# Kernel optimization log

Measured on AMD Instinct MI355X. Metric: run time of the kernel, lower is better.

The kernel has to match this reference:

```python
import jax, jax.numpy as jnp
import numpy as np

EMBED = 1024
HEADS = 16
HEAD_DIM = EMBED // HEADS


def setup_inputs() -> dict:
    key = jax.random.key(0)
    ks = jax.random.split(key, 5)
    s = 0.02
    x = jax.random.normal(ks[0], (2, 2048, EMBED), dtype=jnp.float32)
    W_qkv = jax.random.normal(ks[1], (EMBED, 3 * EMBED), dtype=jnp.float32) * s
    b_qkv = jnp.zeros((3 * EMBED,), dtype=jnp.float32)
    W_proj = jax.random.normal(ks[2], (EMBED, EMBED), dtype=jnp.float32) * s
    b_proj = jnp.zeros((EMBED,), dtype=jnp.float32)
    return {"x": x, "W_qkv": W_qkv, "b_qkv": b_qkv, "W_proj": W_proj, "b_proj": b_proj}


def reference(x, W_qkv, b_qkv, W_proj, b_proj):
    B, N, _ = x.shape
    scale = HEAD_DIM ** -0.5
    qkv = x @ W_qkv + b_qkv                     # [B,N,3E]
    qkv = qkv.reshape(B, N, 3, HEADS, HEAD_DIM)
    q = qkv[:, :, 0].transpose(0, 2, 1, 3) * scale  # [B,H,N,D]
    k = qkv[:, :, 1].transpose(0, 2, 1, 3)
    v = qkv[:, :, 2].transpose(0, 2, 1, 3)
    attn = jnp.einsum('bhnd,bhmd->bhnm', q, k)  # [B,H,N,N]
    attn = jax.nn.softmax(attn, axis=-1)
    out = jnp.einsum('bhnm,bhmd->bhnd', attn, v)  # [B,H,N,D]
    out = out.transpose(0, 2, 1, 3).reshape(B, N, HEADS * HEAD_DIM)
    return out @ W_proj + b_proj
```

## Files before the change

### kernel.cpp

```cpp
#include <hip/hip_runtime.h>
#include <hip/hip_bf16.h>
#include <stdint.h>

typedef unsigned short u16;
typedef __bf16 bf16x8 __attribute__((ext_vector_type(8)));
typedef float f32x4 __attribute__((ext_vector_type(4)));

__device__ __forceinline__ u16 f2bf(float f) {
    union { float f; unsigned u; } x; x.f = f;
    unsigned u = x.u;
    u += 0x7FFFu + ((u >> 16) & 1u);
    return (u16)(u >> 16);
}

typedef __attribute__((address_space(1))) void gvoid;
typedef __attribute__((address_space(3))) void lvoid;
__device__ __forceinline__ void gl2lds16(const void* g, void* l) {
    __builtin_amdgcn_global_load_lds((gvoid*)g, (lvoid*)l, 16, 0, 0);
}

__global__ __launch_bounds__(256) void prep_kernel(
    const float* __restrict__ x, u16* __restrict__ xb,
    const float* __restrict__ Wqkv, u16* __restrict__ wqkvT,
    const float* __restrict__ Wproj, u16* __restrict__ wprojT)
{
    __shared__ u16 tile[64][65];
    const int blk = blockIdx.x;
    const int tid = threadIdx.x;

    if (blk < 2048) {
        const size_t i = ((size_t)blk * 256 + tid) * 8;
        float4 a = *(const float4*)(x + i);
        float4 b = *(const float4*)(x + i + 4);
        ushort4 oa, ob;
        oa.x = f2bf(a.x); oa.y = f2bf(a.y); oa.z = f2bf(a.z); oa.w = f2bf(a.w);
        ob.x = f2bf(b.x); ob.y = f2bf(b.y); ob.z = f2bf(b.z); ob.w = f2bf(b.w);
        *(ushort4*)(xb + i) = oa;
        *(ushort4*)(xb + i + 4) = ob;
        return;
    }
    const float* in; u16* out; int rows, cols, bx, by;
    if (blk < 2816) { int t = blk - 2048; in = Wqkv;  out = wqkvT;  rows = 1024; cols = 3072; bx = t % 48; by = t / 48; }
    else            { int t = blk - 2816; in = Wproj; out = wprojT; rows = 1024; cols = 1024; bx = t % 16; by = t / 16; }
#pragma unroll
    for (int i = 0; i < 16; i++) {
        int e = i * 256 + tid;
        int r = e >> 6, c = e & 63;
        tile[r][c] = f2bf(in[(size_t)(by * 64 + r) * cols + bx * 64 + c]);
    }
    __syncthreads();
#pragma unroll
    for (int i = 0; i < 16; i++) {
        int e = i * 256 + tid;
        int r = e >> 6, c = e & 63;
        out[(size_t)(bx * 64 + r) * rows + by * 64 + c] = tile[c][r];
    }
}

__global__ __launch_bounds__(256) void transpose_v(
    const u16* __restrict__ in, u16* __restrict__ out)
{
    __shared__ u16 tile[64][65];
    const int bh = blockIdx.y;
    const int t0 = blockIdx.x * 64;
    const u16* ip = in + ((size_t)bh * 2048 + t0) * 64;
    u16* op = out + (size_t)bh * 64 * 2048 + t0;
    const int tid = threadIdx.x;
#pragma unroll
    for (int i = 0; i < 16; i++) {
        int e = i * 256 + tid;
        int r = e >> 6, c = e & 63;
        tile[r][c] = ip[(size_t)r * 64 + c];
    }
    __syncthreads();
#pragma unroll
    for (int i = 0; i < 16; i++) {
        int e = i * 256 + tid;
        int d = e >> 6, tt = e & 63;
        op[(size_t)d * 2048 + tt] = tile[tt][d];
    }
}

__global__ __launch_bounds__(256) void gemm_qkv(
    const u16* __restrict__ A, const u16* __restrict__ Bt,
    const float* __restrict__ bias,
    u16* __restrict__ q, u16* __restrict__ ko, u16* __restrict__ vo)
{
    constexpr int K = 1024;
    __shared__ __align__(16) u16 sA[128 * 64];
    __shared__ __align__(16) u16 sB[128 * 64];
    const int tid = threadIdx.x;
    const int wave = tid >> 6, lane = tid & 63;
    const int quad = lane >> 4, l16 = lane & 15;
    const int wm = (wave >> 1) * 64, wn = (wave & 1) * 64;
    const int m0 = blockIdx.y * 128, n0 = blockIdx.x * 128;
    const int srow = lane >> 3;
    const int scol = (lane & 7) * 8;

    f32x4 acc[4][4];
#pragma unroll
    for (int i = 0; i < 4; i++)
#pragma unroll
        for (int j = 0; j < 4; j++)
#pragma unroll
            for (int r = 0; r < 4; r++) acc[i][j][r] = 0.f;

    for (int kt = 0; kt < K; kt += 64) {
        __syncthreads();
#pragma unroll
        for (int t = 0; t < 4; t++) {
            int rb = wave * 32 + t * 8;
            gl2lds16(A  + (size_t)(m0 + rb + srow) * K + kt + scol, &sA[rb * 64]);
            gl2lds16(Bt + (size_t)(n0 + rb + srow) * K + kt + scol, &sB[rb * 64]);
        }
        __syncthreads();
#pragma unroll
        for (int kk = 0; kk < 64; kk += 32) {
            bf16x8 af[4], bfr[4];
#pragma unroll
            for (int t = 0; t < 4; t++) {
                af[t]  = *(const bf16x8*)&sA[(wm + t * 16 + l16) * 64 + kk + quad * 8];
                bfr[t] = *(const bf16x8*)&sB[(wn + t * 16 + l16) * 64 + kk + quad * 8];
            }
#pragma unroll
            for (int i = 0; i < 4; i++)
#pragma unroll
                for (int j = 0; j < 4; j++)
                    acc[i][j] = __builtin_amdgcn_mfma_f32_16x16x32_bf16(
                        af[i], bfr[j], acc[i][j], 0, 0, 0);
        }
    }

    const float QSCALE = 0.18033688011112042f;
#pragma unroll
    for (int i = 0; i < 4; i++) {
#pragma unroll
        for (int j = 0; j < 4; j++) {
            int n = n0 + wn + j * 16 + l16;
            float bv = bias[n];
            int which = n >> 10, rem = n & 1023;
            int h = rem >> 6, d = rem & 63;
#pragma unroll
            for (int r = 0; r < 4; r++) {
                int m = m0 + wm + i * 16 + quad * 4 + r;
                float v = acc[i][j][r] + bv;
                int b = m >> 11, t = m & 2047;
                size_t idx = ((size_t)(b * 16 + h) * 2048 + t) * 64 + d;
                if (which == 0)
                    q[idx] = f2bf(v * QSCALE);
                else if (which == 1)
                    ko[idx] = f2bf(v);
                else
                    vo[idx] = f2bf(v);
            }
        }
    }
}

__global__ __launch_bounds__(256) void attn_kernel(
    const u16* __restrict__ q, const u16* __restrict__ ko,
    const u16* __restrict__ vt, u16* __restrict__ o)
{
    __shared__ __align__(16) u16 sQ[128 * 72];
    __shared__ __align__(16) u16 sK[64 * 72];
    __shared__ __align__(16) u16 sV[80 * 72];
    __shared__ __align__(16) float sPf[128 * 68];

    const int tid = threadIdx.x;
    const int wave = tid >> 6, lane = tid & 63;
    const int quad = lane >> 4, l16 = lane & 15;

    const int lid = blockIdx.x;
    const int xcd = lid & 7, idx = lid >> 3;
    const int h = xcd * 2 + (idx & 1);
    const int b = (idx >> 1) & 1;
    const int q0 = (idx >> 2) * 128;
    const size_t bh = (size_t)(b * 16 + h);

    const u16* qp  = q  + bh * 2048 * 64;
    const u16* kp  = ko + bh * 2048 * 64;
    const u16* vtp = vt + bh * 64 * 2048;

    const int sr0 = tid >> 3;
    const int sc0 = (tid & 7) * 8;
    const int sr1 = (tid + 256) >> 3;
    const int sc1 = sc0;

#pragma unroll
    for (int i = 0; i < 4; i++) {
        int c = tid + i * 256;
        int r = c >> 3, cc = c & 7;
        *(uint4*)&sQ[r * 72 + cc * 8] =
            *(const uint4*)(qp + (size_t)(q0 + r) * 64 + cc * 8);
    }
#pragma unroll
    for (int i = 0; i < 4; i++) {
        int c = tid + i * 256;
        sV[(64 + (c >> 6)) * 72 + (c & 63)] = 0x3F80;
    }

    uint4 pk0 = *(const uint4*)(kp + (size_t)sr0 * 64 + sc0);
    uint4 pk1 = *(const uint4*)(kp + (size_t)sr1 * 64 + sc1);
    uint4 pv0 = *(const uint4*)(vtp + (size_t)sr0 * 2048 + sc0);
    uint4 pv1 = *(const uint4*)(vtp + (size_t)sr1 * 2048 + sc1);

    __syncthreads();

    bf16x8 qf[2][2];
#pragma unroll
    for (int i = 0; i < 2; i++)
#pragma unroll
        for (int k2 = 0; k2 < 2; k2++)
            qf[i][k2] = *(const bf16x8*)&sQ[(wave * 32 + i * 16 + l16) * 72 + k2 * 32 + quad * 8];

    f32x4 accO[2][4];
    f32x4 accL[2];
#pragma unroll
    for (int i = 0; i < 2; i++) {
#pragma unroll
        for (int r = 0; r < 4; r++) accL[i][r] = 0.f;
#pragma unroll
        for (int j = 0; j < 4; j++)
#pragma unroll
            for (int r = 0; r < 4; r++) accO[i][j][r] = 0.f;
    }

    for (int kt = 0; kt < 2048; kt += 64) {
        __syncthreads();
        *(uint4*)&sK[sr0 * 72 + sc0] = pk0;
        *(uint4*)&sK[sr1 * 72 + sc1] = pk1;
        *(uint4*)&sV[sr0 * 72 + sc0] = pv0;
        *(uint4*)&sV[sr1 * 72 + sc1] = pv1;
        if (kt + 64 < 2048) {
            int nt = kt + 64;
            pk0 = *(const uint4*)(kp + (size_t)(nt + sr0) * 64 + sc0);
            pk1 = *(const uint4*)(kp + (size_t)(nt + sr1) * 64 + sc1);
            pv0 = *(const uint4*)(vtp + (size_t)sr0 * 2048 + nt + sc0);
            pv1 = *(const uint4*)(vtp + (size_t)sr1 * 2048 + nt + sc1);
        }
        __syncthreads();

        f32x4 S[2][4];
#pragma unroll
        for (int i = 0; i < 2; i++)
#pragma unroll
            for (int j = 0; j < 4; j++)
#pragma unroll
                for (int r = 0; r < 4; r++) S[i][j][r] = 0.f;
#pragma unroll
        for (int k2 = 0; k2 < 2; k2++) {
            int kk = k2 * 32;
#pragma unroll
            for (int j = 0; j < 4; j++) {
                bf16x8 bk = *(const bf16x8*)&sK[(j * 16 + l16) * 72 + kk + quad * 8];
                S[0][j] = __builtin_amdgcn_mfma_f32_16x16x32_bf16(qf[0][k2], bk, S[0][j], 0, 0, 0);
                S[1][j] = __builtin_amdgcn_mfma_f32_16x16x32_bf16(qf[1][k2], bk, S[1][j], 0, 0, 0);
            }
        }

        float* pw = &sPf[(wave * 32 + quad * 4) * 68 + l16];
#pragma unroll
        for (int i = 0; i < 2; i++)
#pragma unroll
            for (int j = 0; j < 4; j++)
#pragma unroll
                for (int r = 0; r < 4; r++)
                    pw[(i * 16 + r) * 68 + j * 16] = __builtin_amdgcn_exp2f(S[i][j][r]);

#pragma unroll
        for (int k2 = 0; k2 < 2; k2++) {
            int kk = k2 * 32;
            bf16x8 bv[5];
#pragma unroll
            for (int j = 0; j < 5; j++)
                bv[j] = *(const bf16x8*)&sV[(j * 16 + l16) * 72 + kk + quad * 8];
#pragma unroll
            for (int i = 0; i < 2; i++) {
                const uint32_t* pr =
                    (const uint32_t*)&sPf[(wave * 32 + i * 16 + l16) * 68 + kk + quad * 8];
                uint4 w0 = *(const uint4*)pr;
                uint4 w1 = *(const uint4*)(pr + 4);
                union { uint32_t u[4]; bf16x8 v; } ap;
                ap.u[0] = __builtin_amdgcn_perm(w0.y, w0.x, 0x07060302u);
                ap.u[1] = __builtin_amdgcn_perm(w0.w, w0.z, 0x07060302u);
                ap.u[2] = __builtin_amdgcn_perm(w1.y, w1.x, 0x07060302u);
                ap.u[3] = __builtin_amdgcn_perm(w1.w, w1.z, 0x07060302u);
#pragma unroll
                for (int j = 0; j < 4; j++)
                    accO[i][j] = __builtin_amdgcn_mfma_f32_16x16x32_bf16(ap.v, bv[j], accO[i][j], 0, 0, 0);
                accL[i] = __builtin_amdgcn_mfma_f32_16x16x32_bf16(ap.v, bv[4], accL[i], 0, 0, 0);
            }
        }
    }

#pragma unroll
    for (int i = 0; i < 2; i++)
#pragma unroll
        for (int r = 0; r < 4; r++) {
            float inv = 1.f / accL[i][r];
            size_t row = (size_t)b * 2048 + q0 + wave * 32 + i * 16 + quad * 4 + r;
#pragma unroll
            for (int j = 0; j < 4; j++)
                o[row * 1024 + h * 64 + j * 16 + l16] = f2bf(accO[i][j][r] * inv);
        }
}

__global__ __launch_bounds__(256) void gemm_proj(
    const u16* __restrict__ A, const u16* __restrict__ Bt,
    const float* __restrict__ bias, float* __restrict__ out)
{
    constexpr int K = 1024;
    __shared__ __align__(16) u16 sA[128 * 64];
    __shared__ __align__(16) u16 sB[128 * 64];
    const int tid = threadIdx.x;
    const int wave = tid >> 6, lane = tid & 63;
    const int quad = lane >> 4, l16 = lane & 15;
    const int wm = (wave >> 1) * 64, wn = (wave & 1) * 64;
    const int m0 = blockIdx.y * 128, n0 = blockIdx.x * 128;
    const int srow = lane >> 3;
    const int scol = (lane & 7) * 8;

    f32x4 acc[4][4];
#pragma unroll
    for (int i = 0; i < 4; i++)
#pragma unroll
        for (int j = 0; j < 4; j++)
#pragma unroll
            for (int r = 0; r < 4; r++) acc[i][j][r] = 0.f;

    for (int kt = 0; kt < K; kt += 64) {
        __syncthreads();
#pragma unroll
        for (int t = 0; t < 4; t++) {
            int rb = wave * 32 + t * 8;
            gl2lds16(A  + (size_t)(m0 + rb + srow) * K + kt + scol, &sA[rb * 64]);
            gl2lds16(Bt + (size_t)(n0 + rb + srow) * K + kt + scol, &sB[rb * 64]);
        }
        __syncthreads();
#pragma unroll
        for (int kk = 0; kk < 64; kk += 32) {
            bf16x8 af[4], bfr[4];
#pragma unroll
            for (int t = 0; t < 4; t++) {
                af[t]  = *(const bf16x8*)&sA[(wm + t * 16 + l16) * 64 + kk + quad * 8];
                bfr[t] = *(const bf16x8*)&sB[(wn + t * 16 + l16) * 64 + kk + quad * 8];
            }
#pragma unroll
            for (int i = 0; i < 4; i++)
#pragma unroll
                for (int j = 0; j < 4; j++)
                    acc[i][j] = __builtin_amdgcn_mfma_f32_16x16x32_bf16(
                        af[i], bfr[j], acc[i][j], 0, 0, 0);
        }
    }

#pragma unroll
    for (int i = 0; i < 4; i++) {
#pragma unroll
        for (int j = 0; j < 4; j++) {
            int n = n0 + wn + j * 16 + l16;
            float bv = bias[n];
#pragma unroll
            for (int r = 0; r < 4; r++) {
                int m = m0 + wm + i * 16 + quad * 4 + r;
                out[(size_t)m * 1024 + n] = acc[i][j][r] + bv;
            }
        }
    }
}

extern "C" void kernel_launch(void* const* d_in, const int* in_sizes, int n_in,
                              void* d_out, int out_size, void* d_ws, size_t ws_size,
                              hipStream_t stream) {
    const float* x     = (const float*)d_in[0];
    const float* Wqkv  = (const float*)d_in[1];
    const float* bqkv  = (const float*)d_in[2];
    const float* Wproj = (const float*)d_in[3];
    const float* bproj = (const float*)d_in[4];
    float* out = (float*)d_out;
    char* ws = (char*)d_ws;

    u16* wqkvT  = (u16*)(ws);
    u16* wprojT = (u16*)(ws +  6291456);
    u16* xb     = (u16*)(ws +  8388608);
    u16* qb     = (u16*)(ws + 16777216);
    u16* kb     = (u16*)(ws + 25165824);
    u16* vtb    = (u16*)(ws + 33554432);
    u16* ob     = (u16*)(ws + 41943040);
    u16* vb     = ob;

    prep_kernel<<<dim3(3072), 256, 0, stream>>>(x, xb, Wqkv, wqkvT, Wproj, wprojT);
    gemm_qkv<<<dim3(24, 32), 256, 0, stream>>>(xb, wqkvT, bqkv, qb, kb, vb);
    transpose_v<<<dim3(32, 32), 256, 0, stream>>>(vb, vtb);
    attn_kernel<<<dim3(512), 256, 0, stream>>>(qb, kb, vtb, ob);
    gemm_proj<<<dim3(8, 32), 256, 0, stream>>>(ob, wprojT, bproj, out);
}
```

Measured before the change: 222.4 us.

## Register-prefetch GEMM tiles, XCD-aware block mapping, bf16 P in attention

```diff
diff --git a/kernel.cpp b/kernel.cpp
--- a/kernel.cpp
+++ b/kernel.cpp
@@ -11,12 +11,6 @@
     unsigned u = x.u;
     u += 0x7FFFu + ((u >> 16) & 1u);
     return (u16)(u >> 16);
-}
-
-typedef __attribute__((address_space(1))) void gvoid;
-typedef __attribute__((address_space(3))) void lvoid;
-__device__ __forceinline__ void gl2lds16(const void* g, void* l) {
-    __builtin_amdgcn_global_load_lds((gvoid*)g, (lvoid*)l, 16, 0, 0);
 }
 
 __global__ __launch_bounds__(256) void prep_kernel(
@@ -87,15 +81,21 @@
     u16* __restrict__ q, u16* __restrict__ ko, u16* __restrict__ vo)
 {
     constexpr int K = 1024;
-    __shared__ __align__(16) u16 sA[128 * 64];
-    __shared__ __align__(16) u16 sB[128 * 64];
+    __shared__ __align__(16) u16 sA[128 * 72];
+    __shared__ __align__(16) u16 sB[128 * 72];
     const int tid = threadIdx.x;
     const int wave = tid >> 6, lane = tid & 63;
     const int quad = lane >> 4, l16 = lane & 15;
     const int wm = (wave >> 1) * 64, wn = (wave & 1) * 64;
-    const int m0 = blockIdx.y * 128, n0 = blockIdx.x * 128;
-    const int srow = lane >> 3;
-    const int scol = (lane & 7) * 8;
+
+    const int lid = blockIdx.x;
+    const int xcd = lid & 7, idx = lid >> 3;
+    const int sm = xcd & 3, sn = xcd >> 2;
+    const int m0 = (sm * 8 + (idx & 7)) * 128;
+    const int n0 = (sn * 12 + (idx >> 3)) * 128;
+
+    const int srow = tid >> 3;
+    const int scol = (tid & 7) * 8;
 
     f32x4 acc[4][4];
 #pragma unroll
@@ -105,13 +105,27 @@
 #pragma unroll
             for (int r = 0; r < 4; r++) acc[i][j][r] = 0.f;
 
+    uint4 ra[4], rb[4];
+#pragma unroll
+    for (int p = 0; p < 4; p++) {
+        ra[p] = *(const uint4*)(A  + (size_t)(m0 + srow + p * 32) * K + scol);
+        rb[p] = *(const uint4*)(Bt + (size_t)(n0 + srow + p * 32) * K + scol);
+    }
+
     for (int kt = 0; kt < K; kt += 64) {
         __syncthreads();
 #pragma unroll
-        for (int t = 0; t < 4; t++) {
-            int rb = wave * 32 + t * 8;
-            gl2lds16(A  + (size_t)(m0 + rb + srow) * K + kt + scol, &sA[rb * 64]);
-            gl2lds16(Bt + (size_t)(n0 + rb + srow) * K + kt + scol, &sB[rb * 64]);
+        for (int p = 0; p < 4; p++) {
+            *(uint4*)&sA[(srow + p * 32) * 72 + scol] = ra[p];
+            *(uint4*)&sB[(srow + p * 32) * 72 + scol] = rb[p];
+        }
+        if (kt + 64 < K) {
+            int nt = kt + 64;
+#pragma unroll
+            for (int p = 0; p < 4; p++) {
+                ra[p] = *(const uint4*)(A  + (size_t)(m0 + srow + p * 32) * K + nt + scol);
+                rb[p] = *(const uint4*)(Bt + (size_t)(n0 + srow + p * 32) * K + nt + scol);
+            }
         }
         __syncthreads();
 #pragma unroll
@@ -119,8 +133,8 @@
             bf16x8 af[4], bfr[4];
 #pragma unroll
             for (int t = 0; t < 4; t++) {
-                af[t]  = *(const bf16x8*)&sA[(wm + t * 16 + l16) * 64 + kk + quad * 8];
-                bfr[t] = *(const bf16x8*)&sB[(wn + t * 16 + l16) * 64 + kk + quad * 8];
+                af[t]  = *(const bf16x8*)&sA[(wm + t * 16 + l16) * 72 + kk + quad * 8];
+                bfr[t] = *(const bf16x8*)&sB[(wn + t * 16 + l16) * 72 + kk + quad * 8];
             }
 #pragma unroll
             for (int i = 0; i < 4; i++)
@@ -145,13 +159,13 @@
                 int m = m0 + wm + i * 16 + quad * 4 + r;
                 float v = acc[i][j][r] + bv;
                 int b = m >> 11, t = m & 2047;
-                size_t idx = ((size_t)(b * 16 + h) * 2048 + t) * 64 + d;
+                size_t gi = ((size_t)(b * 16 + h) * 2048 + t) * 64 + d;
                 if (which == 0)
-                    q[idx] = f2bf(v * QSCALE);
+                    q[gi] = f2bf(v * QSCALE);
                 else if (which == 1)
-                    ko[idx] = f2bf(v);
+                    ko[gi] = f2bf(v);
                 else
-                    vo[idx] = f2bf(v);
+                    vo[gi] = f2bf(v);
             }
         }
     }
@@ -163,8 +177,8 @@
 {
     __shared__ __align__(16) u16 sQ[128 * 72];
     __shared__ __align__(16) u16 sK[64 * 72];
-    __shared__ __align__(16) u16 sV[80 * 72];
-    __shared__ __align__(16) float sPf[128 * 68];
+    __shared__ __align__(16) u16 sV[64 * 72];
+    __shared__ __align__(16) u16 sP[128 * 72];
 
     const int tid = threadIdx.x;
     const int wave = tid >> 6, lane = tid & 63;
@@ -184,7 +198,6 @@
     const int sr0 = tid >> 3;
     const int sc0 = (tid & 7) * 8;
     const int sr1 = (tid + 256) >> 3;
-    const int sc1 = sc0;
 
 #pragma unroll
     for (int i = 0; i < 4; i++) {
@@ -193,16 +206,14 @@
         *(uint4*)&sQ[r * 72 + cc * 8] =
             *(const uint4*)(qp + (size_t)(q0 + r) * 64 + cc * 8);
     }
-#pragma unroll
-    for (int i = 0; i < 4; i++) {
-        int c = tid + i * 256;
-        sV[(64 + (c >> 6)) * 72 + (c & 63)] = 0x3F80;
-    }
+
+    union { uint32_t u[4]; bf16x8 v; } ones;
+    ones.u[0] = ones.u[1] = ones.u[2] = ones.u[3] = 0x3F803F80u;
 
     uint4 pk0 = *(const uint4*)(kp + (size_t)sr0 * 64 + sc0);
-    uint4 pk1 = *(const uint4*)(kp + (size_t)sr1 * 64 + sc1);
+    uint4 pk1 = *(const uint4*)(kp + (size_t)sr1 * 64 + sc0);
     uint4 pv0 = *(const uint4*)(vtp + (size_t)sr0 * 2048 + sc0);
-    uint4 pv1 = *(const uint4*)(vtp + (size_t)sr1 * 2048 + sc1);
+    uint4 pv1 = *(const uint4*)(vtp + (size_t)sr1 * 2048 + sc0);
 
     __syncthreads();
 
@@ -228,15 +239,15 @@
     for (int kt = 0; kt < 2048; kt += 64) {
         __syncthreads();
         *(uint4*)&sK[sr0 * 72 + sc0] = pk0;
-        *(uint4*)&sK[sr1 * 72 + sc1] = pk1;
+        *(uint4*)&sK[sr1 * 72 + sc0] = pk1;
         *(uint4*)&sV[sr0 * 72 + sc0] = pv0;
-        *(uint4*)&sV[sr1 * 72 + sc1] = pv1;
+        *(uint4*)&sV[sr1 * 72 + sc0] = pv1;
         if (kt + 64 < 2048) {
             int nt = kt + 64;
             pk0 = *(const uint4*)(kp + (size_t)(nt + sr0) * 64 + sc0);
-            pk1 = *(const uint4*)(kp + (size_t)(nt + sr1) * 64 + sc1);
+            pk1 = *(const uint4*)(kp + (size_t)(nt + sr1) * 64 + sc0);
             pv0 = *(const uint4*)(vtp + (size_t)sr0 * 2048 + nt + sc0);
-            pv1 = *(const uint4*)(vtp + (size_t)sr1 * 2048 + nt + sc1);
+            pv1 = *(const uint4*)(vtp + (size_t)sr1 * 2048 + nt + sc0);
         }
         __syncthreads();
 
@@ -258,37 +269,32 @@
             }
         }
 
-        float* pw = &sPf[(wave * 32 + quad * 4) * 68 + l16];
+        u16* pw = &sP[(wave * 32 + quad * 4) * 72 + l16];
 #pragma unroll
         for (int i = 0; i < 2; i++)
 #pragma unroll
             for (int j = 0; j < 4; j++)
 #pragma unroll
-                for (int r = 0; r < 4; r++)
-                    pw[(i * 16 + r) * 68 + j * 16] = __builtin_amdgcn_exp2f(S[i][j][r]);
+                for (int r = 0; r < 4; r++) {
+                    union { float f; uint32_t u; } e;
+                    e.f = __builtin_amdgcn_exp2f(S[i][j][r]);
+                    pw[(i * 16 + r) * 72 + j * 16] = (u16)(e.u >> 16);
+                }
 
 #pragma unroll
         for (int k2 = 0; k2 < 2; k2++) {
             int kk = k2 * 32;
-            bf16x8 bv[5];
-#pragma unroll
-            for (int j = 0; j < 5; j++)
+            bf16x8 bv[4];
+#pragma unroll
+            for (int j = 0; j < 4; j++)
                 bv[j] = *(const bf16x8*)&sV[(j * 16 + l16) * 72 + kk + quad * 8];
 #pragma unroll
             for (int i = 0; i < 2; i++) {
-                const uint32_t* pr =
-                    (const uint32_t*)&sPf[(wave * 32 + i * 16 + l16) * 68 + kk + quad * 8];
-                uint4 w0 = *(const uint4*)pr;
-                uint4 w1 = *(const uint4*)(pr + 4);
-                union { uint32_t u[4]; bf16x8 v; } ap;
-                ap.u[0] = __builtin_amdgcn_perm(w0.y, w0.x, 0x07060302u);
-                ap.u[1] = __builtin_amdgcn_perm(w0.w, w0.z, 0x07060302u);
-                ap.u[2] = __builtin_amdgcn_perm(w1.y, w1.x, 0x07060302u);
-                ap.u[3] = __builtin_amdgcn_perm(w1.w, w1.z, 0x07060302u);
+                bf16x8 ap = *(const bf16x8*)&sP[(wave * 32 + i * 16 + l16) * 72 + kk + quad * 8];
 #pragma unroll
                 for (int j = 0; j < 4; j++)
-                    accO[i][j] = __builtin_amdgcn_mfma_f32_16x16x32_bf16(ap.v, bv[j], accO[i][j], 0, 0, 0);
-                accL[i] = __builtin_amdgcn_mfma_f32_16x16x32_bf16(ap.v, bv[4], accL[i], 0, 0, 0);
+                    accO[i][j] = __builtin_amdgcn_mfma_f32_16x16x32_bf16(ap, bv[j], accO[i][j], 0, 0, 0);
+                accL[i] = __builtin_amdgcn_mfma_f32_16x16x32_bf16(ap, ones.v, accL[i], 0, 0, 0);
             }
         }
     }
@@ -310,15 +316,20 @@
     const float* __restrict__ bias, float* __restrict__ out)
 {
     constexpr int K = 1024;
-    __shared__ __align__(16) u16 sA[128 * 64];
-    __shared__ __align__(16) u16 sB[128 * 64];
+    __shared__ __align__(16) u16 sA[128 * 72];
+    __shared__ __align__(16) u16 sB[128 * 72];
     const int tid = threadIdx.x;
     const int wave = tid >> 6, lane = tid & 63;
     const int quad = lane >> 4, l16 = lane & 15;
     const int wm = (wave >> 1) * 64, wn = (wave & 1) * 64;
-    const int m0 = blockIdx.y * 128, n0 = blockIdx.x * 128;
-    const int srow = lane >> 3;
-    const int scol = (lane & 7) * 8;
+
+    const int lid = blockIdx.x;
+    const int xcd = lid & 7, idx = lid >> 3;
+    const int m0 = (xcd * 4 + (idx >> 3)) * 128;
+    const int n0 = (idx & 7) * 128;
+
+    const int srow = tid >> 3;
+    const int scol = (tid & 7) * 8;
 
     f32x4 acc[4][4];
 #pragma unroll
@@ -328,13 +339,27 @@
 #pragma unroll
             for (int r = 0; r < 4; r++) acc[i][j][r] = 0.f;
 
+    uint4 ra[4], rb[4];
+#pragma unroll
+    for (int p = 0; p < 4; p++) {
+        ra[p] = *(const uint4*)(A  + (size_t)(m0 + srow + p * 32) * K + scol);
+        rb[p] = *(const uint4*)(Bt + (size_t)(n0 + srow + p * 32) * K + scol);
+    }
+
     for (int kt = 0; kt < K; kt += 64) {
         __syncthreads();
 #pragma unroll
-        for (int t = 0; t < 4; t++) {
-            int rb = wave * 32 + t * 8;
-            gl2lds16(A  + (size_t)(m0 + rb + srow) * K + kt + scol, &sA[rb * 64]);
-            gl2lds16(Bt + (size_t)(n0 + rb + srow) * K + kt + scol, &sB[rb * 64]);
+        for (int p = 0; p < 4; p++) {
+            *(uint4*)&sA[(srow + p * 32) * 72 + scol] = ra[p];
+            *(uint4*)&sB[(srow + p * 32) * 72 + scol] = rb[p];
+        }
+        if (kt + 64 < K) {
+            int nt = kt + 64;
+#pragma unroll
+            for (int p = 0; p < 4; p++) {
+                ra[p] = *(const uint4*)(A  + (size_t)(m0 + srow + p * 32) * K + nt + scol);
+                rb[p] = *(const uint4*)(Bt + (size_t)(n0 + srow + p * 32) * K + nt + scol);
+            }
         }
         __syncthreads();
 #pragma unroll
@@ -342,8 +367,8 @@
             bf16x8 af[4], bfr[4];
 #pragma unroll
             for (int t = 0; t < 4; t++) {
-                af[t]  = *(const bf16x8*)&sA[(wm + t * 16 + l16) * 64 + kk + quad * 8];
-                bfr[t] = *(const bf16x8*)&sB[(wn + t * 16 + l16) * 64 + kk + quad * 8];
+                af[t]  = *(const bf16x8*)&sA[(wm + t * 16 + l16) * 72 + kk + quad * 8];
+                bfr[t] = *(const bf16x8*)&sB[(wn + t * 16 + l16) * 72 + kk + quad * 8];
             }
 #pragma unroll
             for (int i = 0; i < 4; i++)
@@ -390,8 +415,8 @@
     u16* vb     = ob;
 
     prep_kernel<<<dim3(3072), 256, 0, stream>>>(x, xb, Wqkv, wqkvT, Wproj, wprojT);
-    gemm_qkv<<<dim3(24, 32), 256, 0, stream>>>(xb, wqkvT, bqkv, qb, kb, vb);
+    gemm_qkv<<<dim3(768), 256, 0, stream>>>(xb, wqkvT, bqkv, qb, kb, vb);
     transpose_v<<<dim3(32, 32), 256, 0, stream>>>(vb, vtb);
     attn_kernel<<<dim3(512), 256, 0, stream>>>(qb, kb, vtb, ob);
-    gemm_proj<<<dim3(8, 32), 256, 0, stream>>>(ob, wprojT, bproj, out);
-}
+    gemm_proj<<<dim3(256), 256, 0, stream>>>(ob, wprojT, bproj, out);
+}
```

New measurement: 310.0 us. +39.4%, slower.
